# Kernel optimization log

Hardware: AMD Instinct MI355X
Metric: run time of the kernel (lower is better)

Reference implementation:

```python
import jax, jax.numpy as jnp
import numpy as np
from jax import lax
from functools import partial

MAX_FRAMES = 12
NUM_SAMPLES = 500
SIGMA = 0.05
TOPK = 49
LN_EPS = 1e-5


def perturbed_topk_indicators(scores, noise, k):
    """scores: (b, d), noise: (b, ns, d) -> indicators (b, k, d).
    Equivalent to one_hot(sorted_topk_indices).mean(samples) without
    materializing the (b, ns, k, d) one-hot tensor (histogram scatter)."""
    b, ns, d = noise.shape
    perturbed = scores[:, None, :] + SIGMA * noise          # (b, ns, d)
    _, idx = lax.top_k(perturbed, k)                        # (b, ns, k)
    idx = jnp.sort(idx, axis=-1)                            # ascending, as in torch code
    # scatter-add counts into (b, k, d)
    flat = (jnp.arange(b)[:, None, None] * k + jnp.arange(k)[None, None, :]) * d + idx
    counts = jnp.zeros(b * k * d, scores.dtype).at[flat.ravel()].add(1.0)
    return counts.reshape(b, k, d) / ns


def reference(x, ln_w, ln_b, w_in, w_out1, w_out2):
    B, L, D = x.shape
    N = L // MAX_FRAMES
    xf = x.reshape(B * MAX_FRAMES, N, D)                    # (Bf, N, D)
    Bf = B * MAX_FRAMES

    # ---- STPredictorConv ----
    mu = xf.mean(-1, keepdims=True)
    var = jnp.var(xf, axis=-1, keepdims=True)
    xn = (xf - mu) * lax.rsqrt(var + LN_EPS) * ln_w + ln_b
    h = jax.nn.gelu(jnp.einsum('bnd,cd->bnc', xn, w_in), approximate=False)  # (Bf, N, C=256)
    C = h.shape[-1]
    g = h[:, :1, :].reshape(B, MAX_FRAMES, 1, C).mean(axis=1, keepdims=True)  # (B,1,1,C)
    g = jnp.broadcast_to(g, (B, MAX_FRAMES, 1, C)).reshape(Bf, 1, C)
    cat = jnp.concatenate([h, jnp.broadcast_to(g, (Bf, N, C))], axis=-1)      # (Bf, N, 2C)
    s = jax.nn.gelu(jnp.einsum('bnd,cd->bnc', cat, w_out1), approximate=False)
    s = jnp.einsum('bnc,oc->bno', s, w_out2)                # (Bf, N, 1)
    score = jax.nn.softmax(s, axis=-1)[..., 0]              # softmax over size-1 dim -> ones; faithful

    # ---- perturbed top-k selection over spatial tokens ----
    spatial_score = score[:, 1:]                            # (Bf, N-1)
    noise = jax.random.normal(jax.random.key(42), (Bf, NUM_SAMPLES, N - 1), x.dtype)
    ind = perturbed_topk_indicators(spatial_score, noise, TOPK)  # (Bf, k, N-1)

    cls_feat = xf[:, :1, :]
    spatial_feat = xf[:, 1:, :]
    selected = jnp.einsum('bkl,bld->bkd', ind, spatial_feat)
    out = jnp.concatenate([cls_feat, selected], axis=1)     # (Bf, 1+k, D)
    return out.reshape(B, MAX_FRAMES * (1 + TOPK), D)


def setup_inputs() -> dict:
    key = jax.random.key(0)
    ks = jax.random.split(key, 4)
    B, N, D, C = 8, 197, 512, 256
    x = jax.random.normal(ks[0], (B, MAX_FRAMES * N, D), jnp.float32)
    return {
        'x': x,
        'ln_w': jnp.ones((D,), jnp.float32),
        'ln_b': jnp.zeros((D,), jnp.float32),
        'w_in': jax.random.normal(ks[1], (C, D), jnp.float32) * 0.02,
        'w_out1': jax.random.normal(ks[2], (C, D), jnp.float32) * 0.02,
        'w_out2': jax.random.normal(ks[3], (1, C), jnp.float32) * 0.02,
    }
```

## Files before the change

kernel.cpp:

```cpp
#include <hip/hip_runtime.h>
#include <stdint.h>

constexpr int BF   = 96;
constexpr int NS   = 500;
constexpr int DSP  = 196;
constexpr int KSEL = 49;
constexpr int NTOK = 197;
constexpr int DIM  = 512;
constexpr int ROWSTRIDE = 64;

__device__ __forceinline__ uint32_t rotl32(uint32_t x, int r) {
  return (x << r) | (x >> (32 - r));
}

__device__ __forceinline__ void threefry2x32(uint32_t x0, uint32_t x1,
                                             uint32_t& o0, uint32_t& o1) {
  const uint32_t ks0 = 0u, ks1 = 42u, ks2 = 0u ^ 42u ^ 0x1BD11BDAu;
  x0 += ks0; x1 += ks1;
#define TF_R(r) { x0 += x1; x1 = rotl32(x1, (r)); x1 ^= x0; }
  TF_R(13) TF_R(15) TF_R(26) TF_R(6)   x0 += ks1; x1 += ks2 + 1u;
  TF_R(17) TF_R(29) TF_R(16) TF_R(24)  x0 += ks2; x1 += ks0 + 2u;
  TF_R(13) TF_R(15) TF_R(26) TF_R(6)   x0 += ks0; x1 += ks1 + 3u;
  TF_R(17) TF_R(29) TF_R(16) TF_R(24)  x0 += ks1; x1 += ks2 + 4u;
  TF_R(13) TF_R(15) TF_R(26) TF_R(6)   x0 += ks2; x1 += ks0 + 5u;
#undef TF_R
  o0 = x0; o1 = x1;
}

__device__ __forceinline__ uint32_t noise_bits(uint32_t p) {
  uint32_t o0, o1;
  threefry2x32(0u, p, o0, o1);
  return o0 ^ o1;
}

__global__ __launch_bounds__(256)
void topk_idx_kernel(uint8_t* __restrict__ idxbuf) {
  const int lane = threadIdx.x & 63;
  const int wid  = (blockIdx.x << 2) | (threadIdx.x >> 6);
  if (wid >= BF * NS) return;
  const uint32_t rowbase = (uint32_t)wid * (uint32_t)DSP;

  uint32_t keys[4];
#pragma unroll
  for (int g = 0; g < 4; ++g) {
    const int j = (g << 6) | lane;
    uint32_t key = 0u;
    if (j < DSP) {
      const uint32_t bits = noise_bits(rowbase + (uint32_t)j);
      key = ((bits >> 9) << 8) | (uint32_t)(DSP - 1 - j);
    }
    keys[g] = key;
  }

  uint32_t T = 0u;
#pragma unroll 1
  for (int bit = 30; bit >= 0; --bit) {
    const uint32_t cand = T | (1u << bit);
    const int c = __popcll(__ballot(keys[0] >= cand))
                + __popcll(__ballot(keys[1] >= cand))
                + __popcll(__ballot(keys[2] >= cand))
                + __popcll(__ballot(keys[3] >= cand));
    if (c >= KSEL) T = cand;
  }

  const uint64_t m0 = __ballot(keys[0] >= T);
  const uint64_t m1 = __ballot(keys[1] >= T);
  const uint64_t m2 = __ballot(keys[2] >= T);
  const uint64_t m3 = __ballot(keys[3] >= T);
  const int c0 = __popcll(m0);
  const int c1 = c0 + __popcll(m1);
  const int c2 = c1 + __popcll(m2);
  const uint64_t below = (1ull << lane) - 1ull;

  uint8_t* row = idxbuf + (size_t)wid * ROWSTRIDE;
  if ((m0 >> lane) & 1ull) row[__popcll(m0 & below)]      = (uint8_t)lane;
  if ((m1 >> lane) & 1ull) row[c0 + __popcll(m1 & below)] = (uint8_t)(64 + lane);
  if ((m2 >> lane) & 1ull) row[c1 + __popcll(m2 & below)] = (uint8_t)(128 + lane);
  if ((m3 >> lane) & 1ull) row[c2 + __popcll(m3 & below)] = (uint8_t)(192 + lane);
}

__global__ __launch_bounds__(512)
void hist_gather_kernel(const float* __restrict__ x,
                        const uint8_t* __restrict__ idxbuf,
                        float* __restrict__ out) {
  const int b = blockIdx.x % BF;
  const int k = blockIdx.x / BF;
  const int d = threadIdx.x;

  __shared__ uint32_t counts[DSP];
  __shared__ uint32_t list[DSP];
  __shared__ uint32_t nnz;

  if (d < DSP) counts[d] = 0u;
  if (d == 0) nnz = 0u;
  __syncthreads();

  if (d < NS) {
    const uint32_t j = idxbuf[(size_t)(b * NS + d) * ROWSTRIDE + k];
    atomicAdd(&counts[j], 1u);
  }
  __syncthreads();

  if (d < DSP) {
    const uint32_t c = counts[d];
    if (c) {
      const uint32_t p = atomicAdd(&nnz, 1u);
      list[p] = (c << 16) | (uint32_t)d;
    }
  }
  __syncthreads();

  const float* xb = x + (size_t)b * NTOK * DIM;
  const int n = (int)nnz;
  float acc = 0.0f;
#pragma unroll 4
  for (int i = 0; i < n; ++i) {
    const uint32_t e = list[i];
    acc = fmaf((float)(e >> 16), xb[(size_t)(1 + (e & 0xffffu)) * DIM + d], acc);
  }

  float* ob = out + (size_t)b * (1 + KSEL) * DIM;
  ob[(size_t)(1 + k) * DIM + d] = acc * (1.0f / (float)NS);
  if (k == 0) ob[d] = xb[d];
}

extern "C" void kernel_launch(void* const* d_in, const int* in_sizes, int n_in,
                              void* d_out, int out_size, void* d_ws, size_t ws_size,
                              hipStream_t stream) {
  const float* x = (const float*)d_in[0];
  float* out = (float*)d_out;
  uint8_t* idxbuf = (uint8_t*)d_ws;

  topk_idx_kernel<<<dim3(BF * NS / 4), 256, 0, stream>>>(idxbuf);
  hist_gather_kernel<<<dim3(BF * KSEL), 512, 0, stream>>>(x, idxbuf, out);
}
```

Measured before the change: 150.3 us.

## Split histogram and gather into per-frame histogram plus dense tiled GEMM

```diff
diff --git a/kernel.cpp b/kernel.cpp
--- a/kernel.cpp
+++ b/kernel.cpp
@@ -8,9 +8,10 @@
 constexpr int NTOK = 197;
 constexpr int DIM  = 512;
 constexpr int ROWSTRIDE = 64;
+constexpr int KROWS = 64;
 
 __device__ __forceinline__ uint32_t rotl32(uint32_t x, int r) {
-  return (x << r) | (x >> (32 - r));
+  return __builtin_amdgcn_alignbit(x, x, 32 - r);
 }
 
 __device__ __forceinline__ void threefry2x32(uint32_t x0, uint32_t x1,
@@ -37,91 +38,144 @@
 void topk_idx_kernel(uint8_t* __restrict__ idxbuf) {
   const int lane = threadIdx.x & 63;
   const int wid  = (blockIdx.x << 2) | (threadIdx.x >> 6);
-  if (wid >= BF * NS) return;
   const uint32_t rowbase = (uint32_t)wid * (uint32_t)DSP;
 
-  uint32_t keys[4];
+  uint32_t m[4];
 #pragma unroll
   for (int g = 0; g < 4; ++g) {
     const int j = (g << 6) | lane;
-    uint32_t key = 0u;
-    if (j < DSP) {
-      const uint32_t bits = noise_bits(rowbase + (uint32_t)j);
-      key = ((bits >> 9) << 8) | (uint32_t)(DSP - 1 - j);
-    }
-    keys[g] = key;
+    uint32_t v = 0u;
+    if (j < DSP) v = noise_bits(rowbase + (uint32_t)j) >> 9;
+    m[g] = v;
   }
 
   uint32_t T = 0u;
 #pragma unroll 1
-  for (int bit = 30; bit >= 0; --bit) {
+  for (int bit = 22; bit >= 0; --bit) {
     const uint32_t cand = T | (1u << bit);
-    const int c = __popcll(__ballot(keys[0] >= cand))
-                + __popcll(__ballot(keys[1] >= cand))
-                + __popcll(__ballot(keys[2] >= cand))
-                + __popcll(__ballot(keys[3] >= cand));
+    const int c = __popcll(__ballot(m[0] >= cand))
+                + __popcll(__ballot(m[1] >= cand))
+                + __popcll(__ballot(m[2] >= cand))
+                + __popcll(__ballot(m[3] >= cand));
     if (c >= KSEL) T = cand;
   }
 
-  const uint64_t m0 = __ballot(keys[0] >= T);
-  const uint64_t m1 = __ballot(keys[1] >= T);
-  const uint64_t m2 = __ballot(keys[2] >= T);
-  const uint64_t m3 = __ballot(keys[3] >= T);
-  const int c0 = __popcll(m0);
-  const int c1 = c0 + __popcll(m1);
-  const int c2 = c1 + __popcll(m2);
+  uint64_t gt[4], eq[4];
+#pragma unroll
+  for (int g = 0; g < 4; ++g) {
+    gt[g] = __ballot(m[g] > T);
+    eq[g] = __ballot(m[g] == T);
+  }
+  eq[3] &= 0xFull;
+
+  const int ngt = __popcll(gt[0]) + __popcll(gt[1]) + __popcll(gt[2]) + __popcll(gt[3]);
+  const int need = KSEL - ngt;
+  const int e0 = __popcll(eq[0]), e1 = __popcll(eq[1]), e2 = __popcll(eq[2]);
   const uint64_t below = (1ull << lane) - 1ull;
 
+  uint64_t fin[4];
+  fin[0] = gt[0] | __ballot(((eq[0] >> lane) & 1ull) &&
+                            (__popcll(eq[0] & below) < need));
+  fin[1] = gt[1] | __ballot(((eq[1] >> lane) & 1ull) &&
+                            (e0 + __popcll(eq[1] & below) < need));
+  fin[2] = gt[2] | __ballot(((eq[2] >> lane) & 1ull) &&
+                            (e0 + e1 + __popcll(eq[2] & below) < need));
+  fin[3] = gt[3] | __ballot(((eq[3] >> lane) & 1ull) &&
+                            (e0 + e1 + e2 + __popcll(eq[3] & below) < need));
+
+  const int c0 = __popcll(fin[0]);
+  const int c1 = c0 + __popcll(fin[1]);
+  const int c2 = c1 + __popcll(fin[2]);
+
   uint8_t* row = idxbuf + (size_t)wid * ROWSTRIDE;
-  if ((m0 >> lane) & 1ull) row[__popcll(m0 & below)]      = (uint8_t)lane;
-  if ((m1 >> lane) & 1ull) row[c0 + __popcll(m1 & below)] = (uint8_t)(64 + lane);
-  if ((m2 >> lane) & 1ull) row[c1 + __popcll(m2 & below)] = (uint8_t)(128 + lane);
-  if ((m3 >> lane) & 1ull) row[c2 + __popcll(m3 & below)] = (uint8_t)(192 + lane);
+  if ((fin[0] >> lane) & 1ull) row[__popcll(fin[0] & below)]      = (uint8_t)lane;
+  if ((fin[1] >> lane) & 1ull) row[c0 + __popcll(fin[1] & below)] = (uint8_t)(64 + lane);
+  if ((fin[2] >> lane) & 1ull) row[c1 + __popcll(fin[2] & below)] = (uint8_t)(128 + lane);
+  if ((fin[3] >> lane) & 1ull) row[c2 + __popcll(fin[3] & below)] = (uint8_t)(192 + lane);
 }
 
 __global__ __launch_bounds__(512)
-void hist_gather_kernel(const float* __restrict__ x,
-                        const uint8_t* __restrict__ idxbuf,
-                        float* __restrict__ out) {
-  const int b = blockIdx.x % BF;
-  const int k = blockIdx.x / BF;
-  const int d = threadIdx.x;
+void hist_kernel(const float* __restrict__ x,
+                 const uint8_t* __restrict__ idxbuf,
+                 uint16_t* __restrict__ cnt,
+                 float* __restrict__ out) {
+  const int b = blockIdx.x;
+  const int t = threadIdx.x;
 
-  __shared__ uint32_t counts[DSP];
-  __shared__ uint32_t list[DSP];
-  __shared__ uint32_t nnz;
-
-  if (d < DSP) counts[d] = 0u;
-  if (d == 0) nnz = 0u;
+  __shared__ uint32_t hist[KSEL * DSP];
+  for (int i = t; i < KSEL * DSP; i += 512) hist[i] = 0u;
   __syncthreads();
 
-  if (d < NS) {
-    const uint32_t j = idxbuf[(size_t)(b * NS + d) * ROWSTRIDE + k];
-    atomicAdd(&counts[j], 1u);
-  }
-  __syncthreads();
-
-  if (d < DSP) {
-    const uint32_t c = counts[d];
-    if (c) {
-      const uint32_t p = atomicAdd(&nnz, 1u);
-      list[p] = (c << 16) | (uint32_t)d;
+  const uint32_t* rows = (const uint32_t*)(idxbuf + (size_t)b * NS * ROWSTRIDE);
+  for (int c = t; c < NS * 4; c += 512) {
+    const int s = c >> 2, part = c & 3;
+    const uint4 v = *(const uint4*)(rows + s * 16 + part * 4);
+    if (part < 3) {
+      const int kbase = part * 16;
+#pragma unroll
+      for (int q = 0; q < 4; ++q) {
+        uint32_t w = (&v.x)[q];
+#pragma unroll
+        for (int bb = 0; bb < 4; ++bb) {
+          atomicAdd(&hist[(kbase + q * 4 + bb) * DSP + (w & 0xffu)], 1u);
+          w >>= 8;
+        }
+      }
+    } else {
+      atomicAdd(&hist[48 * DSP + (v.x & 0xffu)], 1u);
     }
   }
   __syncthreads();
 
-  const float* xb = x + (size_t)b * NTOK * DIM;
-  const int n = (int)nnz;
-  float acc = 0.0f;
-#pragma unroll 4
-  for (int i = 0; i < n; ++i) {
-    const uint32_t e = list[i];
-    acc = fmaf((float)(e >> 16), xb[(size_t)(1 + (e & 0xffffu)) * DIM + d], acc);
+  uint16_t* cb = cnt + (size_t)b * KSEL * DSP;
+  for (int i = t; i < KSEL * DSP; i += 512) cb[i] = (uint16_t)hist[i];
+
+  out[(size_t)b * (1 + KSEL) * DIM + t] = x[(size_t)b * NTOK * DIM + t];
+}
+
+__global__ __launch_bounds__(256)
+void gemm_kernel(const float* __restrict__ x,
+                 const uint16_t* __restrict__ cnt,
+                 float* __restrict__ out) {
+  const int b = blockIdx.x % BF;
+  const int dtile = blockIdx.x / BF;
+  const int t = threadIdx.x;
+  const int dt = t & 15, kg = t >> 4;
+
+  __shared__ float cf[KROWS * DSP];
+  const uint16_t* cb = cnt + (size_t)b * KSEL * DSP;
+  for (int i = t; i < KROWS * DSP; i += 256)
+    cf[i] = (i < KSEL * DSP) ? (float)cb[i] : 0.0f;
+  __syncthreads();
+
+  const float* xb = x + (size_t)b * NTOK * DIM + DIM
+                  + dtile * 64 + dt * 4;
+  float4 acc[4] = {};
+#pragma unroll 1
+  for (int j = 0; j < DSP; ++j) {
+    const float4 xv = *(const float4*)(xb + (size_t)j * DIM);
+#pragma unroll
+    for (int i = 0; i < 4; ++i) {
+      const float c = cf[(kg + 16 * i) * DSP + j];
+      acc[i].x = fmaf(c, xv.x, acc[i].x);
+      acc[i].y = fmaf(c, xv.y, acc[i].y);
+      acc[i].z = fmaf(c, xv.z, acc[i].z);
+      acc[i].w = fmaf(c, xv.w, acc[i].w);
+    }
   }
 
-  float* ob = out + (size_t)b * (1 + KSEL) * DIM;
-  ob[(size_t)(1 + k) * DIM + d] = acc * (1.0f / (float)NS);
-  if (k == 0) ob[d] = xb[d];
+  float* ob = out + (size_t)b * (1 + KSEL) * DIM + dtile * 64 + dt * 4;
+  const float inv = 1.0f / (float)NS;
+#pragma unroll
+  for (int i = 0; i < 4; ++i) {
+    const int k = kg + 16 * i;
+    if (k < KSEL) {
+      float4 r;
+      r.x = acc[i].x * inv; r.y = acc[i].y * inv;
+      r.z = acc[i].z * inv; r.w = acc[i].w * inv;
+      *(float4*)(ob + (size_t)(1 + k) * DIM) = r;
+    }
+  }
 }
 
 extern "C" void kernel_launch(void* const* d_in, const int* in_sizes, int n_in,
@@ -130,7 +184,10 @@
   const float* x = (const float*)d_in[0];
   float* out = (float*)d_out;
   uint8_t* idxbuf = (uint8_t*)d_ws;
+  uint16_t* cnt = (uint16_t*)((uint8_t*)d_ws +
+                              (size_t)BF * NS * ROWSTRIDE);
 
   topk_idx_kernel<<<dim3(BF * NS / 4), 256, 0, stream>>>(idxbuf);
-  hist_gather_kernel<<<dim3(BF * KSEL), 512, 0, stream>>>(x, idxbuf, out);
+  hist_kernel<<<dim3(BF), 512, 0, stream>>>(x, idxbuf, cnt, out);
+  gemm_kernel<<<dim3(BF * 8), 256, 0, stream>>>(x, cnt, out);
 }
```

Measured after the change: 214.4 us. +42.7%, slower.
